# Optimization experiments

Measured on AMD Instinct MI355X. Metric: run time of the kernel, lower is better.

The kernel has to match this reference:

```python
import jax, jax.numpy as jnp
import numpy as np
from jax import lax

DIM = 512; NUM_HEADS = 8; WS = 2; POOL = 3
HEAD_DIM = DIM // NUM_HEADS
L_HEADS = int(NUM_HEADS * 0.5); L_DIM = L_HEADS * HEAD_DIM
H_HEADS = NUM_HEADS - L_HEADS; H_DIM = H_HEADS * HEAD_DIM
SCALE = HEAD_DIM ** (-0.5)


def setup_inputs():
    key = jax.random.key(0)
    ks = jax.random.split(key, 8)
    B, Hh, Ww = 8, 64, 64
    N = Hh * Ww
    s = lambda fan: 1.0 / np.sqrt(fan)
    return {
        'x': jax.random.normal(ks[0], (B, N, DIM), jnp.float32),
        'H': Hh,
        'l_q_w': jax.random.normal(ks[1], (DIM, L_DIM), jnp.float32) * s(DIM),
        'l_kv_w': jax.random.normal(ks[2], (DIM, 2 * L_DIM), jnp.float32) * s(DIM),
        'l_proj_w': jax.random.normal(ks[3], (L_DIM, L_DIM), jnp.float32) * s(L_DIM),
        'l_proj_b': jax.random.normal(ks[4], (L_DIM,), jnp.float32) * 0.01,
        'h_qkv_w': jax.random.normal(ks[5], (DIM, H_DIM), jnp.float32) * s(DIM),
        'h_proj_w': jax.random.normal(ks[6], (H_DIM, H_DIM), jnp.float32) * s(H_DIM),
        'h_proj_b': jax.random.normal(ks[7], (H_DIM,), jnp.float32) * 0.01,
    }


def _avgpool3_same(x):
    # x: [M, ws, ws, C]; 3x3 avg pool, stride 1, pad 1, count_include_pad=False
    ssum = lax.reduce_window(x, jnp.float32(0.0), lax.add,
                             (1, POOL, POOL, 1), (1, 1, 1, 1),
                             ((0, 0), (1, 1), (1, 1), (0, 0)))
    ones = jnp.ones(x.shape[1:3], x.dtype)
    cnt = lax.reduce_window(ones, jnp.float32(0.0), lax.add,
                            (POOL, POOL), (1, 1), ((1, 1), (1, 1)))
    return ssum / cnt[None, :, :, None]


def _hifi(x, h_qkv_w, h_proj_w, h_proj_b):
    B, H, W, C = x.shape
    hg, wg = H // WS, W // WS
    x = x @ h_qkv_w  # [B,H,W,H_DIM]
    # partition into ws x ws windows: [B*hg*wg, ws, ws, H_DIM]
    xw = x.reshape(B, hg, WS, wg, WS, H_DIM).transpose(0, 1, 3, 2, 4, 5)
    xw = xw.reshape(B * hg * wg, WS, WS, H_DIM)
    xw = _avgpool3_same(xw) - xw
    xw = xw.reshape(B, hg, wg, WS, WS, H_DIM).transpose(0, 1, 3, 2, 4, 5)
    xw = xw.reshape(B, H, W, H_DIM)
    return xw @ h_proj_w + h_proj_b


def _lofi(x, l_q_w, l_kv_w, l_proj_w, l_proj_b):
    B, H, W, C = x.shape
    q = (x @ l_q_w).reshape(B, H * W, L_HEADS, HEAD_DIM).transpose(0, 2, 1, 3)
    # spatial reduction: avg pool ws stride ws -> [B, H/ws * W/ws, C]
    xp = x.reshape(B, H // WS, WS, W // WS, WS, C).mean(axis=(2, 4))
    xp = xp.reshape(B, -1, C)
    kv = (xp @ l_kv_w).reshape(B, -1, 2, L_HEADS, HEAD_DIM)
    k = kv[:, :, 0].transpose(0, 2, 1, 3)  # [B,h,M,d]
    v = kv[:, :, 1].transpose(0, 2, 1, 3)
    attn = jax.nn.softmax(jnp.einsum('bhnd,bhmd->bhnm', q, k) * SCALE, axis=-1)
    out = jnp.einsum('bhnm,bhmd->bhnd', attn, v)
    out = out.transpose(0, 2, 1, 3).reshape(B, H, W, L_DIM)
    return out @ l_proj_w + l_proj_b


def reference(x, H, l_q_w, l_kv_w, l_proj_w, l_proj_b, h_qkv_w, h_proj_w, h_proj_b):
    B, N, C = x.shape
    W = N // H
    xg = x.reshape(B, H, W, C)
    hi = _hifi(xg, h_qkv_w, h_proj_w, h_proj_b)
    lo = _lofi(xg, l_q_w, l_kv_w, l_proj_w, l_proj_b)
    out = jnp.concatenate([hi, lo], axis=-1)  # [B,H,W,C]
    return out.reshape(B, N, C)
```

## Files before the change

### kernel.cpp

```cpp
#include <hip/hip_runtime.h>

typedef __bf16 bf16x8 __attribute__((ext_vector_type(8)));
typedef float  f32x4  __attribute__((ext_vector_type(4)));
typedef unsigned int u32x4 __attribute__((ext_vector_type(4)));
typedef unsigned short u16x8 __attribute__((ext_vector_type(8)));
typedef unsigned short u16x4 __attribute__((ext_vector_type(4)));
typedef short i16x4 __attribute__((ext_vector_type(4)));

__device__ __forceinline__ unsigned short f2bf(float f) {
    return __builtin_bit_cast(unsigned short, (__bf16)f);
}
__device__ __forceinline__ float bf2f(unsigned short s) {
    return (float)__builtin_bit_cast(__bf16, s);
}
__device__ __forceinline__ bf16x8 as_bf16x8(u32x4 v) {
    return __builtin_bit_cast(bf16x8, v);
}

#define AS1 __attribute__((address_space(1)))
#define AS3 __attribute__((address_space(3)))
__device__ __forceinline__ void gload_lds16(const void* g, void* l) {
    __builtin_amdgcn_global_load_lds((const AS1 void*)g, (AS3 void*)l, 16, 0, 0);
}


__global__ __launch_bounds__(256) void k_prep(
        const float* __restrict__ x,
        const float* __restrict__ h_qkv_w, const float* __restrict__ l_q_w,
        const float* __restrict__ l_kv_w, const float* __restrict__ h_proj_w,
        const float* __restrict__ l_proj_w,
        unsigned short* __restrict__ xb, unsigned short* __restrict__ xpb,
        unsigned short* __restrict__ wcatT, unsigned short* __restrict__ lkvT,
        unsigned short* __restrict__ hprojT, unsigned short* __restrict__ lprojT) {
    int blk = blockIdx.x;
    if (blk < 8192) {
        int t = blk * 256 + threadIdx.x;
        int row = t >> 6, c8 = (t & 63) << 3;
        int b = row >> 12, nn = row & 4095;
        int hh = nn >> 6, ww = nn & 63;
        int mp = (((b << 10) + ((hh >> 1) << 5) + (ww >> 1)) << 2) + ((hh & 1) << 1) + (ww & 1);
        const float* src = x + (size_t)row * 512 + c8;
        f32x4 v0 = *(const f32x4*)src;
        f32x4 v1 = *(const f32x4*)(src + 4);
        u16x8 o = { f2bf(v0[0]), f2bf(v0[1]), f2bf(v0[2]), f2bf(v0[3]),
                    f2bf(v1[0]), f2bf(v1[1]), f2bf(v1[2]), f2bf(v1[3]) };
        *(u16x8*)(xb + (size_t)mp * 512 + c8) = o;
    } else if (blk < 10240) {
        int t = (blk - 8192) * 256 + threadIdx.x;
        int r = t >> 6, c8 = (t & 63) << 3;
        int b = r >> 10, hw = r & 1023;
        int h2 = hw >> 5, w2 = hw & 31;
        const float* base = x + ((size_t)(b << 12) + (h2 << 7) + (w2 << 1)) * 512 + c8;
        u16x8 o;
#pragma unroll
        for (int half = 0; half < 2; half++) {
            f32x4 a0 = *(const f32x4*)(base + half * 4);
            f32x4 a1 = *(const f32x4*)(base + 512 + half * 4);
            f32x4 a2 = *(const f32x4*)(base + 64 * 512 + half * 4);
            f32x4 a3 = *(const f32x4*)(base + 65 * 512 + half * 4);
            f32x4 m = (a0 + a1 + a2 + a3) * 0.25f;
#pragma unroll
            for (int j = 0; j < 4; j++) o[half * 4 + j] = f2bf(m[j]);
        }
        *(u16x8*)(xpb + (size_t)r * 512 + c8) = o;
    } else {
        int i = (blk - 10240) * 256 + threadIdx.x;
        if (i < 262144) {
            int n = i >> 9, k = i & 511;
            float v = (n < 256) ? h_qkv_w[k * 256 + n] : l_q_w[k * 256 + (n - 256)];
            wcatT[i] = f2bf(v);
        } else if (i < 524288) {
            int j = i - 262144; int n = j >> 9, k = j & 511;
            lkvT[j] = f2bf(l_kv_w[k * 512 + n]);
        } else if (i < 589824) {
            int j = i - 524288; int n = j >> 8, k = j & 255;
            hprojT[j] = f2bf(h_proj_w[k * 256 + n]);
        } else {
            int j = i - 589824; int n = j >> 8, k = j & 255;
            lprojT[j] = f2bf(l_proj_w[k * 256 + n]);
        }
    }
}

__device__ __forceinline__ void mm_core(
        const unsigned short* __restrict__ A, const unsigned short* __restrict__ Bt,
        size_t row0, int col0, int K,
        unsigned short* As, unsigned short* Bs, f32x4 (&acc)[4][4]) {
    const int tid = threadIdx.x;
    const int wave = tid >> 6, lane = tid & 63;
    const int m16 = lane & 15, quad = lane >> 4;
    const int wr = wave >> 1, wc = wave & 1;
    const int srow = lane >> 2;
    const int scol = (lane & 3) * 8;
    const unsigned short* Ap0 = A + (row0 + wave * 32 + srow) * (size_t)K + scol;
    const unsigned short* Ap1 = Ap0 + (size_t)16 * K;
    const unsigned short* Bp0 = Bt + (size_t)(col0 + wave * 32 + srow) * K + scol;
    const unsigned short* Bp1 = Bp0 + (size_t)16 * K;
    unsigned short* Al0 = As + wave * 1024;
    unsigned short* Al1 = As + wave * 1024 + 512;
    unsigned short* Bl0 = Bs + wave * 1024;
    unsigned short* Bl1 = Bs + wave * 1024 + 512;

    for (int k0 = 0; k0 < K; k0 += 32) {
        __syncthreads();
        gload_lds16(Ap0 + k0, Al0);
        gload_lds16(Ap1 + k0, Al1);
        gload_lds16(Bp0 + k0, Bl0);
        gload_lds16(Bp1 + k0, Bl1);
        __syncthreads();
        bf16x8 af[4], bfr[4];
#pragma unroll
        for (int mi = 0; mi < 4; mi++)
            af[mi] = as_bf16x8(*(const u32x4*)(As + (wr * 64 + mi * 16 + m16) * 32 + quad * 8));
#pragma unroll
        for (int ni = 0; ni < 4; ni++)
            bfr[ni] = as_bf16x8(*(const u32x4*)(Bs + (wc * 64 + ni * 16 + m16) * 32 + quad * 8));
#pragma unroll
        for (int mi = 0; mi < 4; mi++)
#pragma unroll
            for (int ni = 0; ni < 4; ni++)
                acc[mi][ni] = __builtin_amdgcn_mfma_f32_16x16x32_bf16(af[mi], bfr[ni], acc[mi][ni], 0, 0, 0);
    }
}

__global__ __launch_bounds__(256, 2) void k_mm512(
        const unsigned short* __restrict__ xb, const unsigned short* __restrict__ xpb,
        const unsigned short* __restrict__ wcatT, const unsigned short* __restrict__ lkvT,
        unsigned short* __restrict__ dbuf, unsigned short* __restrict__ qbuf,
        unsigned short* __restrict__ kbuf, unsigned short* __restrict__ vT) {
    __shared__ __align__(16) unsigned short As[128 * 32];
    __shared__ __align__(16) unsigned short Bs[128 * 32];
    const int flat = blockIdx.x;
    const bool isg1 = flat < 1024;
    const unsigned short* A;
    const unsigned short* Bt;
    size_t row0; int col0;
    if (isg1) { A = xb;  Bt = wcatT; row0 = (size_t)(flat >> 2) * 128; col0 = (flat & 3) * 128; }
    else { int f = flat - 1024; A = xpb; Bt = lkvT; row0 = (size_t)(f >> 2) * 128; col0 = (f & 3) * 128; }

    f32x4 acc[4][4] = {};
    mm_core(A, Bt, row0, col0, 512, As, Bs, acc);

    const int tid = threadIdx.x;
    const int wave = tid >> 6, lane = tid & 63;
    const int m16 = lane & 15, quad = lane >> 4;
    const int wr = wave >> 1, wc = wave & 1;

    if (isg1) {
        if (col0 < 256) {
#pragma unroll
            for (int mi = 0; mi < 4; mi++)
#pragma unroll
                for (int ni = 0; ni < 4; ni++) {
                    const int col = col0 + wc * 64 + ni * 16 + m16;
                    const size_t mb = row0 + wr * 64 + mi * 16 + quad * 4;
                    float v0 = acc[mi][ni][0], v1 = acc[mi][ni][1];
                    float v2 = acc[mi][ni][2], v3 = acc[mi][ni][3];
                    float m = 0.25f * ((v0 + v1) + (v2 + v3));
                    dbuf[(mb + 0) * 256 + col] = f2bf(m - v0);
                    dbuf[(mb + 1) * 256 + col] = f2bf(m - v1);
                    dbuf[(mb + 2) * 256 + col] = f2bf(m - v2);
                    dbuf[(mb + 3) * 256 + col] = f2bf(m - v3);
                }
        } else {
#pragma unroll
            for (int mi = 0; mi < 4; mi++)
#pragma unroll
                for (int ni = 0; ni < 4; ni++) {
                    const int col = col0 - 256 + wc * 64 + ni * 16 + m16;
                    const size_t mb = row0 + wr * 64 + mi * 16 + quad * 4;
#pragma unroll
                    for (int r = 0; r < 4; r++)
                        qbuf[(mb + r) * 256 + col] = f2bf(acc[mi][ni][r]);
                }
        }
    } else {
        if (col0 < 256) {
#pragma unroll
            for (int mi = 0; mi < 4; mi++)
#pragma unroll
                for (int ni = 0; ni < 4; ni++) {
                    const int col = col0 + wc * 64 + ni * 16 + m16;
                    const size_t row = row0 + wr * 64 + mi * 16 + quad * 4;
#pragma unroll
                    for (int r = 0; r < 4; r++)
                        kbuf[(row + r) * 256 + col] = f2bf(acc[mi][ni][r]);
                }
        } else {
#pragma unroll
            for (int mi = 0; mi < 4; mi++)
#pragma unroll
                for (int ni = 0; ni < 4; ni++) {
                    const int d = col0 - 256 + wc * 64 + ni * 16 + m16;
                    const int hh = d >> 6, dd = d & 63;
                    const size_t kvg = row0 + wr * 64 + mi * 16 + quad * 4;
                    const int b = (int)(kvg >> 10), kv = (int)(kvg & 1023);
                    u16x4 pk = { f2bf(acc[mi][ni][0]), f2bf(acc[mi][ni][1]),
                                 f2bf(acc[mi][ni][2]), f2bf(acc[mi][ni][3]) };
                    *(u16x4*)(vT + (((size_t)(b * 4 + hh) * 64 + dd) << 10) + kv) = pk;
                }
        }
    }
}

__global__ __launch_bounds__(256, 2) void k_mmproj(
        const unsigned short* __restrict__ dbuf, const unsigned short* __restrict__ aout,
        const unsigned short* __restrict__ hprojT, const unsigned short* __restrict__ lprojT,
        const float* __restrict__ h_proj_b, const float* __restrict__ l_proj_b,
        float* __restrict__ out) {
    __shared__ __align__(16) unsigned short As[128 * 32];
    __shared__ __align__(16) unsigned short Bs[128 * 32];
    const int flat = blockIdx.x;
    const bool hi = flat < 512;
    const int f = flat & 511;
    const unsigned short* A  = hi ? dbuf : aout;
    const unsigned short* Bt = hi ? hprojT : lprojT;
    const float* bias = hi ? h_proj_b : l_proj_b;
    const int coloff = hi ? 0 : 256;
    const size_t row0 = (size_t)(f >> 1) * 128;
    const int col0 = (f & 1) * 128;

    f32x4 acc[4][4] = {};
    mm_core(A, Bt, row0, col0, 256, As, Bs, acc);

    const int tid = threadIdx.x;
    const int wave = tid >> 6, lane = tid & 63;
    const int m16 = lane & 15, quad = lane >> 4;
    const int wr = wave >> 1, wc = wave & 1;

#pragma unroll
    for (int mi = 0; mi < 4; mi++)
#pragma unroll
        for (int ni = 0; ni < 4; ni++) {
            const int col = col0 + wc * 64 + ni * 16 + m16;
            const float bv = bias[col];
            const size_t mb = row0 + wr * 64 + mi * 16 + quad * 4;
            const int widx = (int)(mb >> 2);
            const int b = widx >> 10, rem = widx & 1023;
            const int h2 = rem >> 5, w2 = rem & 31;
            const size_t nb = ((size_t)b << 12) + (h2 << 7) + (w2 << 1);
            float* op = out + nb * 512 + coloff + col;
            op[0]            = acc[mi][ni][0] + bv;
            op[512]          = acc[mi][ni][1] + bv;
            op[64 * 512]     = acc[mi][ni][2] + bv;
            op[65 * 512]     = acc[mi][ni][3] + bv;
        }
}

__global__ __launch_bounds__(256, 2) void k_attn(
        const unsigned short* __restrict__ qbuf,
        const unsigned short* __restrict__ kbuf,
        const unsigned short* __restrict__ vT,
        unsigned short* __restrict__ aout) {
    __shared__ __align__(16) unsigned short Kb[2][64 * 72];
    __shared__ __align__(16) unsigned short Vb[2][64 * 72];
    const int tid = threadIdx.x;
    const int wave = tid >> 6, lane = tid & 63;
    const int m16 = lane & 15, quad = lane >> 4;
    const int qtile = blockIdx.x, bh = blockIdx.y;
    const int b = bh >> 2, h = bh & 3;

    bf16x8 qf[4][2];
    const size_t qrow0 = (size_t)b * 4096 + qtile * 256 + wave * 64;
#pragma unroll
    for (int qh = 0; qh < 4; qh++) {
        const unsigned short* qp = qbuf + (qrow0 + qh * 16 + m16) * 256 + h * 64 + quad * 8;
        qf[qh][0] = as_bf16x8(*(const u32x4*)qp);
        qf[qh][1] = as_bf16x8(*(const u32x4*)(qp + 32));
    }

    f32x4 o[4][4] = {};
    float lp[4] = {0.f, 0.f, 0.f, 0.f};

    const int sr = tid >> 3;
    const int sc = tid & 7;
    const unsigned short* kg = kbuf + ((size_t)b * 1024) * 256 + h * 64 + sc * 8;
    const unsigned short* vg = vT + ((size_t)bh * 64) * 1024 + sc * 8;

    u32x4 s0 = *(const u32x4*)(kg + (size_t)sr * 256);
    u32x4 s1 = *(const u32x4*)(kg + (size_t)(sr + 32) * 256);
    u32x4 s2 = *(const u32x4*)(vg + (size_t)sr * 1024);
    u32x4 s3 = *(const u32x4*)(vg + (size_t)(sr + 32) * 1024);
    *(u32x4*)&Kb[0][sr * 72 + sc * 8] = s0;
    *(u32x4*)&Kb[0][(sr + 32) * 72 + sc * 8] = s1;
    *(u32x4*)&Vb[0][sr * 72 + sc * 8] = s2;
    *(u32x4*)&Vb[0][(sr + 32) * 72 + sc * 8] = s3;

    for (int it = 0; it < 16; ++it) {
        const int cur = it & 1, nxt = cur ^ 1;
        __syncthreads();
        if (it + 1 < 16) {
            const size_t kvb = (size_t)(it + 1) * 64;
            s0 = *(const u32x4*)(kg + (kvb + sr) * 256);
            s1 = *(const u32x4*)(kg + (kvb + sr + 32) * 256);
            s2 = *(const u32x4*)(vg + kvb + (size_t)sr * 1024);
            s3 = *(const u32x4*)(vg + kvb + (size_t)(sr + 32) * 1024);
        }

#pragma unroll
        for (int mt = 0; mt < 4; mt++) {
            const unsigned short* kp = &Kb[cur][(mt * 16 + m16) * 72 + quad * 8];
            const bf16x8 kf0 = as_bf16x8(*(const u32x4*)kp);
            const bf16x8 kf1 = as_bf16x8(*(const u32x4*)(kp + 32));
            f32x4 st[4];
#pragma unroll
            for (int qh = 0; qh < 4; qh++) {
                f32x4 z = {};
                z = __builtin_amdgcn_mfma_f32_16x16x32_bf16(kf0, qf[qh][0], z, 0, 0, 0);
                st[qh] = __builtin_amdgcn_mfma_f32_16x16x32_bf16(kf1, qf[qh][1], z, 0, 0, 0);
            }
            i16x4 pa[4];
#pragma unroll
            for (int qh = 0; qh < 4; qh++) {
                float p0 = __expf(st[qh][0] * 0.125f);
                float p1 = __expf(st[qh][1] * 0.125f);
                float p2 = __expf(st[qh][2] * 0.125f);
                float p3 = __expf(st[qh][3] * 0.125f);
                lp[qh] += (p0 + p1) + (p2 + p3);
                u16x4 pk = { f2bf(p0), f2bf(p1), f2bf(p2), f2bf(p3) };
                pa[qh] = __builtin_bit_cast(i16x4, pk);
            }
#pragma unroll
            for (int nt = 0; nt < 4; nt++) {
                const i16x4 vb = *(const i16x4*)&Vb[cur][(nt * 16 + m16) * 72 + mt * 16 + quad * 4];
#pragma unroll
                for (int qh = 0; qh < 4; qh++)
                    o[qh][nt] = __builtin_amdgcn_mfma_f32_16x16x16bf16_1k(pa[qh], vb, o[qh][nt], 0, 0, 0);
            }
        }

        if (it + 1 < 16) {
            *(u32x4*)&Kb[nxt][sr * 72 + sc * 8] = s0;
            *(u32x4*)&Kb[nxt][(sr + 32) * 72 + sc * 8] = s1;
            *(u32x4*)&Vb[nxt][sr * 72 + sc * 8] = s2;
            *(u32x4*)&Vb[nxt][(sr + 32) * 72 + sc * 8] = s3;
        }
    }

#pragma unroll
    for (int qh = 0; qh < 4; qh++) {
        float l = lp[qh];
        l += __shfl_xor(l, 16);
        l += __shfl_xor(l, 32);
        f32x4 linv;
#pragma unroll
        for (int r = 0; r < 4; r++)
            linv[r] = __builtin_amdgcn_rcpf(__shfl(l, quad * 4 + r));
#pragma unroll
        for (int nt = 0; nt < 4; nt++)
#pragma unroll
            for (int r = 0; r < 4; r++)
                aout[(qrow0 + qh * 16 + quad * 4 + r) * 256 + h * 64 + nt * 16 + m16] =
                    f2bf(o[qh][nt][r] * linv[r]);
    }
}


extern "C" void kernel_launch(void* const* d_in, const int* in_sizes, int n_in,
                              void* d_out, int out_size, void* d_ws, size_t ws_size,
                              hipStream_t stream) {
    (void)in_sizes; (void)n_in; (void)out_size; (void)ws_size;
    const float* x        = (const float*)d_in[0];
    const float* l_q_w    = (const float*)d_in[2];
    const float* l_kv_w   = (const float*)d_in[3];
    const float* l_proj_w = (const float*)d_in[4];
    const float* l_proj_b = (const float*)d_in[5];
    const float* h_qkv_w  = (const float*)d_in[6];
    const float* h_proj_w = (const float*)d_in[7];
    const float* h_proj_b = (const float*)d_in[8];
    float* out = (float*)d_out;

    char* ws = (char*)d_ws;
    unsigned short* xb     = (unsigned short*)(ws);
    unsigned short* aout   = (unsigned short*)(ws);
    unsigned short* dbuf   = (unsigned short*)(ws + 33554432);
    unsigned short* qbuf   = (unsigned short*)(ws + 50331648);
    unsigned short* kbuf   = (unsigned short*)(ws + 67108864);
    unsigned short* vT     = (unsigned short*)(ws + 71303168);
    unsigned short* xpb    = (unsigned short*)(ws + 75497472);
    unsigned short* wcatT  = (unsigned short*)(ws + 83886080);
    unsigned short* lkvT   = (unsigned short*)(ws + 84410368);
    unsigned short* hprojT = (unsigned short*)(ws + 84934656);
    unsigned short* lprojT = (unsigned short*)(ws + 85065728);

    k_prep<<<12800, 256, 0, stream>>>(x, h_qkv_w, l_q_w, l_kv_w, h_proj_w, l_proj_w,
                                      xb, xpb, wcatT, lkvT, hprojT, lprojT);
    k_mm512<<<1280, 256, 0, stream>>>(xb, xpb, wcatT, lkvT, dbuf, qbuf, kbuf, vT);
    k_attn<<<dim3(16, 32), 256, 0, stream>>>(qbuf, kbuf, vT, aout);
    k_mmproj<<<1024, 256, 0, stream>>>(dbuf, aout, hprojT, lprojT, h_proj_b, l_proj_b, out);
}
```

Baseline: 249.1 us.

## Fuse x conversion with pooling, remap blocks across XCDs, fold softmax scale into Q

The prep kernel now reads each 2x2 window of x once and writes both the permuted bf16 copy and the pooled average, instead of reading x twice in separate block ranges. Block IDs in both GEMM kernels are remapped so that neighbouring tiles land on the same XCD, aiming for better L2 reuse of the A/B panels. The softmax scale times log2(e) is folded into Q when it is stored, so attention uses exp2 with no extra multiply. Folding the scale before the bf16 rounding of Q slightly changes numerics.

```diff
diff --git a/kernel.cpp b/kernel.cpp
--- a/kernel.cpp
+++ b/kernel.cpp
@@ -9,9 +9,6 @@
 
 __device__ __forceinline__ unsigned short f2bf(float f) {
     return __builtin_bit_cast(unsigned short, (__bf16)f);
-}
-__device__ __forceinline__ float bf2f(unsigned short s) {
-    return (float)__builtin_bit_cast(__bf16, s);
 }
 __device__ __forceinline__ bf16x8 as_bf16x8(u32x4 v) {
     return __builtin_bit_cast(bf16x8, v);
@@ -33,38 +30,30 @@
         unsigned short* __restrict__ wcatT, unsigned short* __restrict__ lkvT,
         unsigned short* __restrict__ hprojT, unsigned short* __restrict__ lprojT) {
     int blk = blockIdx.x;
-    if (blk < 8192) {
+    if (blk < 2048) {
         int t = blk * 256 + threadIdx.x;
-        int row = t >> 6, c8 = (t & 63) << 3;
-        int b = row >> 12, nn = row & 4095;
-        int hh = nn >> 6, ww = nn & 63;
-        int mp = (((b << 10) + ((hh >> 1) << 5) + (ww >> 1)) << 2) + ((hh & 1) << 1) + (ww & 1);
-        const float* src = x + (size_t)row * 512 + c8;
-        f32x4 v0 = *(const f32x4*)src;
-        f32x4 v1 = *(const f32x4*)(src + 4);
-        u16x8 o = { f2bf(v0[0]), f2bf(v0[1]), f2bf(v0[2]), f2bf(v0[3]),
-                    f2bf(v1[0]), f2bf(v1[1]), f2bf(v1[2]), f2bf(v1[3]) };
-        *(u16x8*)(xb + (size_t)mp * 512 + c8) = o;
-    } else if (blk < 10240) {
-        int t = (blk - 8192) * 256 + threadIdx.x;
-        int r = t >> 6, c8 = (t & 63) << 3;
-        int b = r >> 10, hw = r & 1023;
-        int h2 = hw >> 5, w2 = hw & 31;
+        int widx = t >> 6, c8 = (t & 63) << 3;
+        int b = widx >> 10, rem = widx & 1023;
+        int h2 = rem >> 5, w2 = rem & 31;
         const float* base = x + ((size_t)(b << 12) + (h2 << 7) + (w2 << 1)) * 512 + c8;
-        u16x8 o;
-#pragma unroll
-        for (int half = 0; half < 2; half++) {
-            f32x4 a0 = *(const f32x4*)(base + half * 4);
-            f32x4 a1 = *(const f32x4*)(base + 512 + half * 4);
-            f32x4 a2 = *(const f32x4*)(base + 64 * 512 + half * 4);
-            f32x4 a3 = *(const f32x4*)(base + 65 * 512 + half * 4);
-            f32x4 m = (a0 + a1 + a2 + a3) * 0.25f;
-#pragma unroll
-            for (int j = 0; j < 4; j++) o[half * 4 + j] = f2bf(m[j]);
-        }
-        *(u16x8*)(xpb + (size_t)r * 512 + c8) = o;
+        f32x4 acc0 = {}, acc1 = {};
+        const int roff[4] = {0, 1, 64, 65};
+#pragma unroll
+        for (int j = 0; j < 4; j++) {
+            const float* src = base + (size_t)roff[j] * 512;
+            f32x4 v0 = *(const f32x4*)src;
+            f32x4 v1 = *(const f32x4*)(src + 4);
+            acc0 += v0; acc1 += v1;
+            u16x8 o = { f2bf(v0[0]), f2bf(v0[1]), f2bf(v0[2]), f2bf(v0[3]),
+                        f2bf(v1[0]), f2bf(v1[1]), f2bf(v1[2]), f2bf(v1[3]) };
+            *(u16x8*)(xb + ((size_t)widx * 4 + j) * 512 + c8) = o;
+        }
+        acc0 *= 0.25f; acc1 *= 0.25f;
+        u16x8 p = { f2bf(acc0[0]), f2bf(acc0[1]), f2bf(acc0[2]), f2bf(acc0[3]),
+                    f2bf(acc1[0]), f2bf(acc1[1]), f2bf(acc1[2]), f2bf(acc1[3]) };
+        *(u16x8*)(xpb + (size_t)widx * 512 + c8) = p;
     } else {
-        int i = (blk - 10240) * 256 + threadIdx.x;
+        int i = (blk - 2048) * 256 + threadIdx.x;
         if (i < 262144) {
             int n = i >> 9, k = i & 511;
             float v = (n < 256) ? h_qkv_w[k * 256 + n] : l_q_w[k * 256 + (n - 256)];
@@ -130,7 +119,8 @@
         unsigned short* __restrict__ kbuf, unsigned short* __restrict__ vT) {
     __shared__ __align__(16) unsigned short As[128 * 32];
     __shared__ __align__(16) unsigned short Bs[128 * 32];
-    const int flat = blockIdx.x;
+    const int bid = blockIdx.x;
+    const int flat = (bid & 7) * 160 + (bid >> 3);
     const bool isg1 = flat < 1024;
     const unsigned short* A;
     const unsigned short* Bt;
@@ -171,7 +161,7 @@
                     const size_t mb = row0 + wr * 64 + mi * 16 + quad * 4;
 #pragma unroll
                     for (int r = 0; r < 4; r++)
-                        qbuf[(mb + r) * 256 + col] = f2bf(acc[mi][ni][r]);
+                        qbuf[(mb + r) * 256 + col] = f2bf(acc[mi][ni][r] * 0.18033688f);
                 }
         }
     } else {
@@ -210,7 +200,8 @@
         float* __restrict__ out) {
     __shared__ __align__(16) unsigned short As[128 * 32];
     __shared__ __align__(16) unsigned short Bs[128 * 32];
-    const int flat = blockIdx.x;
+    const int bid = blockIdx.x;
+    const int flat = (bid & 7) * 128 + (bid >> 3);
     const bool hi = flat < 512;
     const int f = flat & 511;
     const unsigned short* A  = hi ? dbuf : aout;
@@ -312,10 +303,10 @@
             i16x4 pa[4];
 #pragma unroll
             for (int qh = 0; qh < 4; qh++) {
-                float p0 = __expf(st[qh][0] * 0.125f);
-                float p1 = __expf(st[qh][1] * 0.125f);
-                float p2 = __expf(st[qh][2] * 0.125f);
-                float p3 = __expf(st[qh][3] * 0.125f);
+                float p0 = __builtin_exp2f(st[qh][0]);
+                float p1 = __builtin_exp2f(st[qh][1]);
+                float p2 = __builtin_exp2f(st[qh][2]);
+                float p3 = __builtin_exp2f(st[qh][3]);
                 lp[qh] += (p0 + p1) + (p2 + p3);
                 u16x4 pk = { f2bf(p0), f2bf(p1), f2bf(p2), f2bf(p3) };
                 pa[qh] = __builtin_bit_cast(i16x4, pk);
@@ -383,8 +374,8 @@
     unsigned short* hprojT = (unsigned short*)(ws + 84934656);
     unsigned short* lprojT = (unsigned short*)(ws + 85065728);
 
-    k_prep<<<12800, 256, 0, stream>>>(x, h_qkv_w, l_q_w, l_kv_w, h_proj_w, l_proj_w,
-                                      xb, xpb, wcatT, lkvT, hprojT, lprojT);
+    k_prep<<<4608, 256, 0, stream>>>(x, h_qkv_w, l_q_w, l_kv_w, h_proj_w, l_proj_w,
+                                     xb, xpb, wcatT, lkvT, hprojT, lprojT);
     k_mm512<<<1280, 256, 0, stream>>>(xb, xpb, wcatT, lkvT, dbuf, qbuf, kbuf, vT);
     k_attn<<<dim3(16, 32), 256, 0, stream>>>(qbuf, kbuf, vT, aout);
     k_mmproj<<<1024, 256, 0, stream>>>(dbuf, aout, hprojT, lprojT, h_proj_b, l_proj_b, out);
```

New measurement: 242.6 us. 1.03x faster.
